# Performance work log

Measured on AMD Instinct MI355X. Metric: run time of the kernel, lower is better.

The kernel has to match this reference:

```python
import jax, jax.numpy as jnp
import numpy as np
import math

EPS = 1e-5

def _ln(x):
    # LayerNorm over last dim, no affine (elementwise_affine=False)
    m = jnp.mean(x, axis=-1, keepdims=True)
    v = jnp.var(x, axis=-1, keepdims=True)
    return (x - m) / jnp.sqrt(v + EPS)

def setup_inputs() -> dict:
    key = jax.random.key(0)
    ks = jax.random.split(key, 12)
    bs, P, L, D, H, V = 32, 256, 32, 128, 128, 300
    std = 1.0 / math.sqrt(H)
    xav = math.sqrt(2.0 / ((V + 1) + D))
    emb = jax.random.normal(ks[2], (V + 1, D), jnp.float32) * xav
    emb = emb.at[V].set(0.0)  # padding_idx row
    u = lambda k, shp: jax.random.uniform(k, shp, jnp.float32, -std, std)
    return {
        "paths": jax.random.randint(ks[0], (bs, P, L), 0, V + 1),
        "paths_mask": jax.random.randint(ks[1], (bs, P), 1, L + 1),
        "emb": emb,
        "Wi": u(ks[3], (2 * H, D)), "bi": u(ks[4], (2 * H,)),
        "Wh": u(ks[5], (2 * H, H)), "bh": u(ks[6], (2 * H,)),
        "Ww": u(ks[7], (H, D)), "bw": u(ks[8], (H,)),
        "Wu": u(ks[9], (H, H)), "bu": u(ks[10], (H,)),
        "gamma": jnp.ones((2 * H,), jnp.float32),
        "beta": jnp.zeros((2 * H,), jnp.float32),
    }

def reference(paths, paths_mask, emb, Wi, bi, Wh, bh, Ww, bw, Wu, bu, gamma, beta):
    bs, P, L = paths.shape
    D = emb.shape[1]
    H = Ww.shape[0]
    B = bs * P
    # Embed and flatten paths: [L, B, D] (time-major for scan)
    x = emb[paths].reshape(B * L and (B, L, D))  # [B, L, D]
    x = jnp.transpose(x, (1, 0, 2))              # [L, B, D]
    # Input-dependent parts precomputed across all timesteps
    xi = _ln(jnp.einsum('lbd,gd->lbg', x, Wi) + bi)  # [L, B, 2H]
    xw = _ln(jnp.einsum('lbd,hd->lbh', x, Ww) + bw)  # [L, B, H]

    def step(h, xs_t):
        i2h_t, xw_t = xs_t
        h2h = _ln(h @ Wh.T + bh)
        gates = jax.nn.sigmoid(i2h_t + h2h)
        z = gates[:, :H]
        r = gates[:, H:]
        hu = _ln(h @ Wu.T + bu)
        h_hat = jnp.tanh(xw_t + r * hu)
        h_new = (1.0 - z) * h + z * h_hat
        return h_new, h_new

    h0 = jnp.zeros((B, H), x.dtype)
    _, ys = jax.lax.scan(step, h0, (xi, xw))      # ys: [L, B, H]
    lengths = paths_mask.reshape(-1)              # [B]
    out = ys[lengths - 1, jnp.arange(B)]          # [B, H] hidden at last valid step
    out = out.reshape(bs, P, H)
    # interleave forward/backward halves (relation-path pairing)
    fwd = jnp.concatenate([out[:, 0::2, :], out[:, 1::2, :]], axis=-1)
    bwd = jnp.concatenate([out[:, 1::2, :], out[:, 0::2, :]], axis=-1)
    res = jnp.zeros((bs, P, 2 * H), out.dtype)
    res = res.at[:, 0::2, :].set(fwd).at[:, 1::2, :].set(bwd)
    # final affine LayerNorm (gru_ln)
    m = jnp.mean(res, axis=-1, keepdims=True)
    v = jnp.var(res, axis=-1, keepdims=True)
    return (res - m) / jnp.sqrt(v + EPS) * gamma + beta
```

## Files before the change

kernel.cpp:

```cpp
#include <hip/hip_runtime.h>

typedef float  f32x4 __attribute__((ext_vector_type(4)));
typedef short  s16x8 __attribute__((ext_vector_type(8)));

__device__ __forceinline__ unsigned short bfb(float x) {
  unsigned u = __builtin_bit_cast(unsigned, x);
  return (unsigned short)((u + 0x7FFFu + ((u >> 16) & 1u)) >> 16);
}
__device__ __forceinline__ float fast_sig(float x) {
  float e = __builtin_amdgcn_exp2f(x * -1.44269504f);
  return __builtin_amdgcn_rcpf(1.f + e);
}
__device__ __forceinline__ float fast_tanh(float x) {
  float e = __builtin_amdgcn_exp2f(x * 2.88539008f);
  return 1.f - 2.f * __builtin_amdgcn_rcpf(1.f + e);
}

__global__ __launch_bounds__(256) void tab_kernel(
    const float* __restrict__ emb,
    const float* __restrict__ Wi, const float* __restrict__ bi,
    const float* __restrict__ Ww, const float* __restrict__ bw,
    const float* __restrict__ Wh, const float* __restrict__ Wu,
    const int* __restrict__ pmask, int* __restrict__ perm,
    float* __restrict__ xi_tab, float* __restrict__ xw_tab,
    s16x8* __restrict__ frags)
{
  if (blockIdx.x == 309) {
    __shared__ int hist[33];
    __shared__ int base2[33];
    const int tid = threadIdx.x;
    if (tid < 33) hist[tid] = 0;
    __syncthreads();
    for (int i = tid; i < 8192; i += 256) atomicAdd(&hist[pmask[i]], 1);
    __syncthreads();
    if (tid == 0) {
      int acc = 0;
      for (int l = 1; l <= 32; ++l) { base2[l] = acc; acc += hist[l]; }
    }
    __syncthreads();
    for (int i = tid; i < 8192; i += 256) {
      const int pos = atomicAdd(&base2[pmask[i]], 1);
      perm[pos] = i;
    }
    return;
  }
  if (blockIdx.x >= 301) {
    const int T = blockIdx.x - 301;
    const int lane = threadIdx.x;
    if (lane >= 64) return;
    const int a = lane & 15, s = lane >> 4;
    const float* rowp[3];
    rowp[0] = Wh + (16 * T + a) * 128;
    rowp[1] = Wh + (128 + 16 * T + a) * 128;
    rowp[2] = Wu + (16 * T + a) * 128;
    #pragma unroll
    for (int mat = 0; mat < 3; ++mat) {
      #pragma unroll
      for (int kk = 0; kk < 4; ++kk) {
        const float* src = rowp[mat] + 32 * kk + 8 * s;
        const float4 A = *(const float4*)src;
        const float4 B = *(const float4*)(src + 4);
        s16x8 v;
        v[0] = (short)bfb(A.x); v[1] = (short)bfb(A.y);
        v[2] = (short)bfb(A.z); v[3] = (short)bfb(A.w);
        v[4] = (short)bfb(B.x); v[5] = (short)bfb(B.y);
        v[6] = (short)bfb(B.z); v[7] = (short)bfb(B.w);
        frags[((mat * 8 + T) * 4 + kk) * 64 + lane] = v;
      }
    }
    return;
  }

  const int v = blockIdx.x;
  const int g = threadIdx.x;
  const float4* er = (const float4*)(emb + v * 128);

  float acc = bi[g];
  const float4* wr = (const float4*)(Wi + g * 128);
  #pragma unroll 8
  for (int j = 0; j < 32; ++j) {
    float4 e = er[j], w4 = wr[j];
    acc = fmaf(e.x, w4.x, acc); acc = fmaf(e.y, w4.y, acc);
    acc = fmaf(e.z, w4.z, acc); acc = fmaf(e.w, w4.w, acc);
  }
  float accw = 0.f;
  if (g < 128) {
    accw = bw[g];
    const float4* wr2 = (const float4*)(Ww + g * 128);
    #pragma unroll 8
    for (int j = 0; j < 32; ++j) {
      float4 e = er[j], w4 = wr2[j];
      accw = fmaf(e.x, w4.x, accw); accw = fmaf(e.y, w4.y, accw);
      accw = fmaf(e.z, w4.z, accw); accw = fmaf(e.w, w4.w, accw);
    }
  }
  __shared__ float rs[4][2], rw[2][2];
  float s = acc, q = acc * acc;
  #pragma unroll
  for (int m = 1; m < 64; m <<= 1) { s += __shfl_xor(s, m); q += __shfl_xor(q, m); }
  if ((threadIdx.x & 63) == 0) { rs[threadIdx.x >> 6][0] = s; rs[threadIdx.x >> 6][1] = q; }
  float sw_ = accw, qw_ = accw * accw;
  #pragma unroll
  for (int m = 1; m < 64; m <<= 1) { sw_ += __shfl_xor(sw_, m); qw_ += __shfl_xor(qw_, m); }
  if (g < 128 && (g & 63) == 0) { rw[g >> 6][0] = sw_; rw[g >> 6][1] = qw_; }
  __syncthreads();
  const float SH = rs[0][0] + rs[1][0] + rs[2][0] + rs[3][0];
  const float QH = rs[0][1] + rs[1][1] + rs[2][1] + rs[3][1];
  const float mH = SH * (1.f / 256.f);
  const float rH = rsqrtf(fmaxf(QH * (1.f / 256.f) - mH * mH, 0.f) + 1e-5f);
  xi_tab[v * 256 + g] = (acc - mH) * rH;
  if (g < 128) {
    const float SW = rw[0][0] + rw[1][0], QW = rw[0][1] + rw[1][1];
    const float mW = SW * (1.f / 128.f);
    const float rW = rsqrtf(fmaxf(QW * (1.f / 128.f) - mW * mW, 0.f) + 1e-5f);
    xw_tab[v * 128 + g] = (accw - mW) * rW;
  }
}

__global__ __launch_bounds__(256, 2) void rec_kernel(
    const int* __restrict__ paths, const int* __restrict__ pmask,
    const int* __restrict__ perm,
    const float* __restrict__ bh, const float* __restrict__ bu,
    const float* __restrict__ xi_tab, const float* __restrict__ xw_tab,
    const s16x8* __restrict__ frags,
    float* __restrict__ out)
{
  __shared__ unsigned char hbuf[4096];
  __shared__ alignas(16) float red[4][4][16][4];
  __shared__ int plT[512];

  const int tid  = threadIdx.x;
  const int w    = tid >> 6;
  const int lane = tid & 63;
  const int s    = lane >> 4;
  const int r    = lane & 15;
  const int grp  = (blockIdx.x < 256) ? blockIdx.x : 767 - blockIdx.x;
  const int base = grp * 16;
  const int gb0  = 32 * w + 4 * s;

  s16x8 wz[2][4], wr2[2][4], wu2[2][4];
  #pragma unroll
  for (int u = 0; u < 2; ++u) {
    const int T = 2 * w + u;
    #pragma unroll
    for (int kk = 0; kk < 4; ++kk) {
      wz[u][kk]  = frags[((0 * 8 + T) * 4 + kk) * 64 + lane];
      wr2[u][kk] = frags[((1 * 8 + T) * 4 + kk) * 64 + lane];
      wu2[u][kk] = frags[((2 * 8 + T) * 4 + kk) * 64 + lane];
    }
  }

  for (int k = tid; k < 512; k += 256)
    plT[(k >> 4) * 16 + (k & 15)] = paths[perm[base + (k & 15)] * 32 + (k >> 4)];
  ((uint4*)hbuf)[tid] = uint4{0u, 0u, 0u, 0u};

  const int ri  = perm[base + r];
  const int len = pmask[ri];
  const int len_max = __shfl(len, 15);

  f32x4 bz[2], br2[2], bu2[2];
  #pragma unroll
  for (int u = 0; u < 2; ++u) {
    bz[u]  = *(const f32x4*)(bh + gb0 + 16 * u);
    br2[u] = *(const f32x4*)(bh + 128 + gb0 + 16 * u);
    bu2[u] = *(const f32x4*)(bu + gb0 + 16 * u);
  }

  int hoff[4];
  #pragma unroll
  for (int kk = 0; kk < 4; ++kk)
    hoff[kk] = r * 256 + (((4 * kk + s) ^ r) << 4);
  int hwadr[2];
  #pragma unroll
  for (int u = 0; u < 2; ++u)
    hwadr[u] = r * 256 + (((4 * w + 2 * u + (s >> 1)) ^ r) << 4) + (s & 1) * 8;

  float hreg[2][4] = {{0.f, 0.f, 0.f, 0.f}, {0.f, 0.f, 0.f, 0.f}};
  float* orow = out + (size_t)ri * 256 + gb0;

  __syncthreads();

  f32x4 xiz[2], xir[2], xwv[2];
  {
    const int p = plT[r];
    #pragma unroll
    for (int u = 0; u < 2; ++u) {
      xiz[u] = *(const f32x4*)(xi_tab + p * 256 + gb0 + 16 * u);
      xir[u] = *(const f32x4*)(xi_tab + p * 256 + 128 + gb0 + 16 * u);
      xwv[u] = *(const f32x4*)(xw_tab + p * 128 + gb0 + 16 * u);
    }
  }

  #pragma unroll 1
  for (int t = 0; t < len_max; ++t) {
    const int tn = (t + 1 < len_max) ? t + 1 : t;
    const int pn = plT[tn * 16 + r];
    f32x4 nxiz[2], nxir[2], nxwv[2];
    #pragma unroll
    for (int u = 0; u < 2; ++u) {
      nxiz[u] = *(const f32x4*)(xi_tab + pn * 256 + gb0 + 16 * u);
      nxir[u] = *(const f32x4*)(xi_tab + pn * 256 + 128 + gb0 + 16 * u);
      nxwv[u] = *(const f32x4*)(xw_tab + pn * 128 + gb0 + 16 * u);
    }

    f32x4 az[2] = {}, ar[2] = {}, au[2] = {};
    #pragma unroll
    for (int kk = 0; kk < 4; ++kk) {
      const s16x8 hb = *(const s16x8*)(hbuf + hoff[kk]);
      #pragma unroll
      for (int u = 0; u < 2; ++u) {
        az[u] = __builtin_amdgcn_mfma_f32_16x16x32_bf16(wz[u][kk],  hb, az[u], 0, 0, 0);
        ar[u] = __builtin_amdgcn_mfma_f32_16x16x32_bf16(wr2[u][kk], hb, ar[u], 0, 0, 0);
        au[u] = __builtin_amdgcn_mfma_f32_16x16x32_bf16(wu2[u][kk], hb, au[u], 0, 0, 0);
      }
    }

    float sH = 0.f, qH = 0.f, sU = 0.f, qU = 0.f;
    #pragma unroll
    for (int u = 0; u < 2; ++u) {
      #pragma unroll
      for (int i = 0; i < 4; ++i) {
        az[u][i] += bz[u][i];  sH += az[u][i]; qH = fmaf(az[u][i], az[u][i], qH);
        ar[u][i] += br2[u][i]; sH += ar[u][i]; qH = fmaf(ar[u][i], ar[u][i], qH);
        au[u][i] += bu2[u][i]; sU += au[u][i]; qU = fmaf(au[u][i], au[u][i], qU);
      }
    }
    *(f32x4*)&red[w][s][r][0] = f32x4{sH, qH, sU, qU};

    __syncthreads();

    f32x4 acc0 = *(const f32x4*)&red[0][0][r][0];
    f32x4 acc1 = *(const f32x4*)&red[0][1][r][0];
    #pragma unroll
    for (int c = 2; c < 16; c += 2) {
      acc0 += *(const f32x4*)&red[c >> 2][c & 3][r][0];
      acc1 += *(const f32x4*)&red[(c + 1) >> 2][(c + 1) & 3][r][0];
    }
    const f32x4 S = acc0 + acc1;
    const float mH = S[0] * (1.f / 256.f);
    const float rsH = rsqrtf(fmaxf(S[1] * (1.f / 256.f) - mH * mH, 0.f) + 1e-5f);
    const float cH = -mH * rsH;
    const float mU = S[2] * (1.f / 128.f);
    const float rsU = rsqrtf(fmaxf(S[3] * (1.f / 128.f) - mU * mU, 0.f) + 1e-5f);
    const float cU = -mU * rsU;

    float hn[2][4];
    #pragma unroll
    for (int u = 0; u < 2; ++u) {
      #pragma unroll
      for (int i = 0; i < 4; ++i) {
        const float zg = fast_sig(xiz[u][i] + fmaf(az[u][i], rsH, cH));
        const float rg = fast_sig(xir[u][i] + fmaf(ar[u][i], rsH, cH));
        const float hu = fmaf(au[u][i], rsU, cU);
        const float hh = fast_tanh(fmaf(rg, hu, xwv[u][i]));
        hn[u][i] = fmaf(zg, hh - hreg[u][i], hreg[u][i]);
      }
    }
    if (t == len - 1) {
      #pragma unroll
      for (int u = 0; u < 2; ++u)
        *(float4*)(orow + 16 * u) = float4{hn[u][0], hn[u][1], hn[u][2], hn[u][3]};
    }

    #pragma unroll
    for (int u = 0; u < 2; ++u) {
      const unsigned lo  = (unsigned)bfb(hn[u][0]) | ((unsigned)bfb(hn[u][1]) << 16);
      const unsigned hi2 = (unsigned)bfb(hn[u][2]) | ((unsigned)bfb(hn[u][3]) << 16);
      *(uint2*)(hbuf + hwadr[u]) = uint2{lo, hi2};
      #pragma unroll
      for (int i = 0; i < 4; ++i) hreg[u][i] = hn[u][i];
      xiz[u] = nxiz[u]; xir[u] = nxir[u]; xwv[u] = nxwv[u];
    }
    __syncthreads();
  }
}

__global__ __launch_bounds__(256) void out_kernel(
    const float* __restrict__ gamma, const float* __restrict__ beta,
    float* __restrict__ out)
{
  const int tid = threadIdx.x;
  const int lane = tid & 63;
  const int m = blockIdx.x * 4 + (tid >> 6);
  float* pa = out + (size_t)(2 * m) * 256;
  float* pb = pa + 256;
  const float oa0 = pa[lane], oa1 = pa[64 + lane];
  const float ob0 = pb[lane], ob1 = pb[64 + lane];
  float s = oa0 + oa1 + ob0 + ob1;
  float q = oa0 * oa0 + oa1 * oa1 + ob0 * ob0 + ob1 * ob1;
  #pragma unroll
  for (int msk = 1; msk < 64; msk <<= 1) { s += __shfl_xor(s, msk); q += __shfl_xor(q, msk); }
  const float mean = s * (1.f / 256.f);
  const float rstd = rsqrtf(fmaxf(q * (1.f / 256.f) - mean * mean, 0.f) + 1e-5f);
  const float g0 = gamma[lane], g1 = gamma[64 + lane], g2 = gamma[128 + lane], g3 = gamma[192 + lane];
  const float b0 = beta[lane],  b1 = beta[64 + lane],  b2 = beta[128 + lane],  b3 = beta[192 + lane];
  const float na0 = (oa0 - mean) * rstd, na1 = (oa1 - mean) * rstd;
  const float nb0 = (ob0 - mean) * rstd, nb1 = (ob1 - mean) * rstd;
  pa[lane]       = na0 * g0 + b0;
  pa[64 + lane]  = na1 * g1 + b1;
  pa[128 + lane] = nb0 * g2 + b2;
  pa[192 + lane] = nb1 * g3 + b3;
  pb[lane]       = nb0 * g0 + b0;
  pb[64 + lane]  = nb1 * g1 + b1;
  pb[128 + lane] = na0 * g2 + b2;
  pb[192 + lane] = na1 * g3 + b3;
}

extern "C" void kernel_launch(void* const* d_in, const int* in_sizes, int n_in,
                              void* d_out, int out_size, void* d_ws, size_t ws_size,
                              hipStream_t stream) {
  const int*   paths = (const int*)d_in[0];
  const int*   pmask = (const int*)d_in[1];
  const float* emb   = (const float*)d_in[2];
  const float* Wi    = (const float*)d_in[3];
  const float* bi    = (const float*)d_in[4];
  const float* Wh    = (const float*)d_in[5];
  const float* bh    = (const float*)d_in[6];
  const float* Ww    = (const float*)d_in[7];
  const float* bw    = (const float*)d_in[8];
  const float* Wu    = (const float*)d_in[9];
  const float* bu    = (const float*)d_in[10];
  const float* gamma = (const float*)d_in[11];
  const float* beta  = (const float*)d_in[12];
  float* out = (float*)d_out;

  float* xi_tab = (float*)d_ws;
  float* xw_tab = xi_tab + 301 * 256;
  s16x8* frags  = (s16x8*)((char*)d_ws + 462336);
  int*   perm   = (int*)((char*)d_ws + 560640);

  hipLaunchKernelGGL(tab_kernel, dim3(310), dim3(256), 0, stream,
                     emb, Wi, bi, Ww, bw, Wh, Wu, pmask, perm, xi_tab, xw_tab, frags);
  hipLaunchKernelGGL(rec_kernel, dim3(512), dim3(256), 0, stream,
                     paths, pmask, perm, bh, bu, xi_tab, xw_tab, frags, out);
  hipLaunchKernelGGL(out_kernel, dim3(1024), dim3(256), 0, stream, gamma, beta, out);
}
```

Baseline: 75.17 us.

## Run GRU recurrence with one wavefront per block, weights split between registers and LDS

Each 16-path group is now handled by a single 64-lane wavefront instead of four. Wu fragments stay in registers, while the Wh z/r fragments are staged in LDS and read every step. The LayerNorm reduction moves from shared memory plus block barriers to wave shuffles, removing per-step __syncthreads. The trade-off is that each wave issues four times as many MFMAs serially per step, the xi/xw prefetch for the next step is gone, and 73 KB of LDS per block limits how many blocks fit on a CU.

```diff
diff --git a/kernel.cpp b/kernel.cpp
--- a/kernel.cpp
+++ b/kernel.cpp
@@ -2,6 +2,8 @@
 
 typedef float  f32x4 __attribute__((ext_vector_type(4)));
 typedef short  s16x8 __attribute__((ext_vector_type(8)));
+
+#define REC_LDS_BYTES 73216
 
 __device__ __forceinline__ unsigned short bfb(float x) {
   unsigned u = __builtin_bit_cast(unsigned, x);
@@ -117,7 +119,7 @@
   }
 }
 
-__global__ __launch_bounds__(256, 2) void rec_kernel(
+__global__ __launch_bounds__(64, 1) void rec_kernel(
     const int* __restrict__ paths, const int* __restrict__ pmask,
     const int* __restrict__ perm,
     const float* __restrict__ bh, const float* __restrict__ bu,
@@ -125,153 +127,142 @@
     const s16x8* __restrict__ frags,
     float* __restrict__ out)
 {
-  __shared__ unsigned char hbuf[4096];
-  __shared__ alignas(16) float red[4][4][16][4];
-  __shared__ int plT[512];
-
-  const int tid  = threadIdx.x;
-  const int w    = tid >> 6;
-  const int lane = tid & 63;
+  extern __shared__ char smem[];
+  s16x8* wlds = (s16x8*)smem;
+  unsigned char* hbuf = (unsigned char*)(smem + 65536);
+  float* blds = (float*)(smem + 69632);
+  int* plT = (int*)(smem + 71168);
+
+  const int lane = threadIdx.x;
   const int s    = lane >> 4;
   const int r    = lane & 15;
   const int grp  = (blockIdx.x < 256) ? blockIdx.x : 767 - blockIdx.x;
   const int base = grp * 16;
-  const int gb0  = 32 * w + 4 * s;
-
-  s16x8 wz[2][4], wr2[2][4], wu2[2][4];
-  #pragma unroll
-  for (int u = 0; u < 2; ++u) {
-    const int T = 2 * w + u;
-    #pragma unroll
-    for (int kk = 0; kk < 4; ++kk) {
-      wz[u][kk]  = frags[((0 * 8 + T) * 4 + kk) * 64 + lane];
-      wr2[u][kk] = frags[((1 * 8 + T) * 4 + kk) * 64 + lane];
-      wu2[u][kk] = frags[((2 * 8 + T) * 4 + kk) * 64 + lane];
-    }
-  }
-
-  for (int k = tid; k < 512; k += 256)
+
+  #pragma unroll 4
+  for (int i = 0; i < 64; ++i)
+    wlds[i * 64 + lane] = frags[i * 64 + lane];
+  s16x8 wu[8][4];
+  #pragma unroll
+  for (int T = 0; T < 8; ++T)
+    #pragma unroll
+    for (int kk = 0; kk < 4; ++kk)
+      wu[T][kk] = frags[((16 + T) * 4 + kk) * 64 + lane];
+  #pragma unroll
+  for (int i = 0; i < 4; ++i) blds[lane + 64 * i] = bh[lane + 64 * i];
+  #pragma unroll
+  for (int i = 0; i < 2; ++i) blds[256 + lane + 64 * i] = bu[lane + 64 * i];
+  {
+    uint4 z{0u, 0u, 0u, 0u};
+    #pragma unroll
+    for (int i = 0; i < 4; ++i) ((uint4*)hbuf)[i * 64 + lane] = z;
+  }
+  #pragma unroll
+  for (int k0 = 0; k0 < 512; k0 += 64) {
+    const int k = k0 + lane;
     plT[(k >> 4) * 16 + (k & 15)] = paths[perm[base + (k & 15)] * 32 + (k >> 4)];
-  ((uint4*)hbuf)[tid] = uint4{0u, 0u, 0u, 0u};
+  }
 
   const int ri  = perm[base + r];
   const int len = pmask[ri];
   const int len_max = __shfl(len, 15);
 
-  f32x4 bz[2], br2[2], bu2[2];
-  #pragma unroll
-  for (int u = 0; u < 2; ++u) {
-    bz[u]  = *(const f32x4*)(bh + gb0 + 16 * u);
-    br2[u] = *(const f32x4*)(bh + 128 + gb0 + 16 * u);
-    bu2[u] = *(const f32x4*)(bu + gb0 + 16 * u);
-  }
-
   int hoff[4];
   #pragma unroll
   for (int kk = 0; kk < 4; ++kk)
     hoff[kk] = r * 256 + (((4 * kk + s) ^ r) << 4);
-  int hwadr[2];
-  #pragma unroll
-  for (int u = 0; u < 2; ++u)
-    hwadr[u] = r * 256 + (((4 * w + 2 * u + (s >> 1)) ^ r) << 4) + (s & 1) * 8;
-
-  float hreg[2][4] = {{0.f, 0.f, 0.f, 0.f}, {0.f, 0.f, 0.f, 0.f}};
-  float* orow = out + (size_t)ri * 256 + gb0;
-
-  __syncthreads();
-
-  f32x4 xiz[2], xir[2], xwv[2];
-  {
-    const int p = plT[r];
-    #pragma unroll
-    for (int u = 0; u < 2; ++u) {
-      xiz[u] = *(const f32x4*)(xi_tab + p * 256 + gb0 + 16 * u);
-      xir[u] = *(const f32x4*)(xi_tab + p * 256 + 128 + gb0 + 16 * u);
-      xwv[u] = *(const f32x4*)(xw_tab + p * 128 + gb0 + 16 * u);
-    }
-  }
+  int hwadr[8];
+  #pragma unroll
+  for (int T = 0; T < 8; ++T)
+    hwadr[T] = r * 256 + (((2 * T + (s >> 1)) ^ r) << 4) + (s & 1) * 8;
+
+  f32x4 hold[8];
+  #pragma unroll
+  for (int T = 0; T < 8; ++T) hold[T] = f32x4{0.f, 0.f, 0.f, 0.f};
+
+  float* orow = out + (size_t)ri * 256 + 4 * s;
 
   #pragma unroll 1
   for (int t = 0; t < len_max; ++t) {
-    const int tn = (t + 1 < len_max) ? t + 1 : t;
-    const int pn = plT[tn * 16 + r];
-    f32x4 nxiz[2], nxir[2], nxwv[2];
-    #pragma unroll
-    for (int u = 0; u < 2; ++u) {
-      nxiz[u] = *(const f32x4*)(xi_tab + pn * 256 + gb0 + 16 * u);
-      nxir[u] = *(const f32x4*)(xi_tab + pn * 256 + 128 + gb0 + 16 * u);
-      nxwv[u] = *(const f32x4*)(xw_tab + pn * 128 + gb0 + 16 * u);
-    }
-
-    f32x4 az[2] = {}, ar[2] = {}, au[2] = {};
-    #pragma unroll
-    for (int kk = 0; kk < 4; ++kk) {
-      const s16x8 hb = *(const s16x8*)(hbuf + hoff[kk]);
-      #pragma unroll
-      for (int u = 0; u < 2; ++u) {
-        az[u] = __builtin_amdgcn_mfma_f32_16x16x32_bf16(wz[u][kk],  hb, az[u], 0, 0, 0);
-        ar[u] = __builtin_amdgcn_mfma_f32_16x16x32_bf16(wr2[u][kk], hb, ar[u], 0, 0, 0);
-        au[u] = __builtin_amdgcn_mfma_f32_16x16x32_bf16(wu2[u][kk], hb, au[u], 0, 0, 0);
+    const int p = plT[t * 16 + r];
+
+    s16x8 hb[4];
+    #pragma unroll
+    for (int kk = 0; kk < 4; ++kk)
+      hb[kk] = *(const s16x8*)(hbuf + hoff[kk]);
+
+    f32x4 az[8], ar[8], au[8];
+    #pragma unroll
+    for (int T = 0; T < 8; ++T) {
+      az[T] = *(const f32x4*)&blds[16 * T + 4 * s];
+      ar[T] = *(const f32x4*)&blds[128 + 16 * T + 4 * s];
+      au[T] = *(const f32x4*)&blds[256 + 16 * T + 4 * s];
+    }
+    #pragma unroll
+    for (int kk = 0; kk < 4; ++kk)
+      #pragma unroll
+      for (int T = 0; T < 8; ++T)
+        au[T] = __builtin_amdgcn_mfma_f32_16x16x32_bf16(wu[T][kk], hb[kk], au[T], 0, 0, 0);
+    #pragma unroll
+    for (int T = 0; T < 8; ++T)
+      #pragma unroll
+      for (int kk = 0; kk < 4; ++kk)
+        az[T] = __builtin_amdgcn_mfma_f32_16x16x32_bf16(wlds[(T * 4 + kk) * 64 + lane], hb[kk], az[T], 0, 0, 0);
+    #pragma unroll
+    for (int T = 0; T < 8; ++T)
+      #pragma unroll
+      for (int kk = 0; kk < 4; ++kk)
+        ar[T] = __builtin_amdgcn_mfma_f32_16x16x32_bf16(wlds[((8 + T) * 4 + kk) * 64 + lane], hb[kk], ar[T], 0, 0, 0);
+
+    f32x4 xiz[8], xir[8], xwv[8];
+    #pragma unroll
+    for (int T = 0; T < 8; ++T) {
+      xiz[T] = *(const f32x4*)(xi_tab + p * 256 + 16 * T + 4 * s);
+      xir[T] = *(const f32x4*)(xi_tab + p * 256 + 128 + 16 * T + 4 * s);
+      xwv[T] = *(const f32x4*)(xw_tab + p * 128 + 16 * T + 4 * s);
+    }
+
+    float sH = 0.f, qH = 0.f, sU = 0.f, qU = 0.f;
+    #pragma unroll
+    for (int T = 0; T < 8; ++T) {
+      #pragma unroll
+      for (int i = 0; i < 4; ++i) {
+        sH += az[T][i]; qH = fmaf(az[T][i], az[T][i], qH);
+        sH += ar[T][i]; qH = fmaf(ar[T][i], ar[T][i], qH);
+        sU += au[T][i]; qU = fmaf(au[T][i], au[T][i], qU);
       }
     }
-
-    float sH = 0.f, qH = 0.f, sU = 0.f, qU = 0.f;
-    #pragma unroll
-    for (int u = 0; u < 2; ++u) {
+    sH += __shfl_xor(sH, 16); qH += __shfl_xor(qH, 16);
+    sU += __shfl_xor(sU, 16); qU += __shfl_xor(qU, 16);
+    sH += __shfl_xor(sH, 32); qH += __shfl_xor(qH, 32);
+    sU += __shfl_xor(sU, 32); qU += __shfl_xor(qU, 32);
+
+    const float mH = sH * (1.f / 256.f);
+    const float rsH = rsqrtf(fmaxf(qH * (1.f / 256.f) - mH * mH, 0.f) + 1e-5f);
+    const float cH = -mH * rsH;
+    const float mU = sU * (1.f / 128.f);
+    const float rsU = rsqrtf(fmaxf(qU * (1.f / 128.f) - mU * mU, 0.f) + 1e-5f);
+    const float cU = -mU * rsU;
+
+    const bool emit = (t == len - 1);
+    #pragma unroll
+    for (int T = 0; T < 8; ++T) {
+      f32x4 hn;
       #pragma unroll
       for (int i = 0; i < 4; ++i) {
-        az[u][i] += bz[u][i];  sH += az[u][i]; qH = fmaf(az[u][i], az[u][i], qH);
-        ar[u][i] += br2[u][i]; sH += ar[u][i]; qH = fmaf(ar[u][i], ar[u][i], qH);
-        au[u][i] += bu2[u][i]; sU += au[u][i]; qU = fmaf(au[u][i], au[u][i], qU);
+        const float zg = fast_sig(xiz[T][i] + fmaf(az[T][i], rsH, cH));
+        const float rg = fast_sig(xir[T][i] + fmaf(ar[T][i], rsH, cH));
+        const float hu = fmaf(au[T][i], rsU, cU);
+        const float hh = fast_tanh(fmaf(rg, hu, xwv[T][i]));
+        hn[i] = fmaf(zg, hh - hold[T][i], hold[T][i]);
       }
-    }
-    *(f32x4*)&red[w][s][r][0] = f32x4{sH, qH, sU, qU};
-
-    __syncthreads();
-
-    f32x4 acc0 = *(const f32x4*)&red[0][0][r][0];
-    f32x4 acc1 = *(const f32x4*)&red[0][1][r][0];
-    #pragma unroll
-    for (int c = 2; c < 16; c += 2) {
-      acc0 += *(const f32x4*)&red[c >> 2][c & 3][r][0];
-      acc1 += *(const f32x4*)&red[(c + 1) >> 2][(c + 1) & 3][r][0];
-    }
-    const f32x4 S = acc0 + acc1;
-    const float mH = S[0] * (1.f / 256.f);
-    const float rsH = rsqrtf(fmaxf(S[1] * (1.f / 256.f) - mH * mH, 0.f) + 1e-5f);
-    const float cH = -mH * rsH;
-    const float mU = S[2] * (1.f / 128.f);
-    const float rsU = rsqrtf(fmaxf(S[3] * (1.f / 128.f) - mU * mU, 0.f) + 1e-5f);
-    const float cU = -mU * rsU;
-
-    float hn[2][4];
-    #pragma unroll
-    for (int u = 0; u < 2; ++u) {
-      #pragma unroll
-      for (int i = 0; i < 4; ++i) {
-        const float zg = fast_sig(xiz[u][i] + fmaf(az[u][i], rsH, cH));
-        const float rg = fast_sig(xir[u][i] + fmaf(ar[u][i], rsH, cH));
-        const float hu = fmaf(au[u][i], rsU, cU);
-        const float hh = fast_tanh(fmaf(rg, hu, xwv[u][i]));
-        hn[u][i] = fmaf(zg, hh - hreg[u][i], hreg[u][i]);
-      }
-    }
-    if (t == len - 1) {
-      #pragma unroll
-      for (int u = 0; u < 2; ++u)
-        *(float4*)(orow + 16 * u) = float4{hn[u][0], hn[u][1], hn[u][2], hn[u][3]};
-    }
-
-    #pragma unroll
-    for (int u = 0; u < 2; ++u) {
-      const unsigned lo  = (unsigned)bfb(hn[u][0]) | ((unsigned)bfb(hn[u][1]) << 16);
-      const unsigned hi2 = (unsigned)bfb(hn[u][2]) | ((unsigned)bfb(hn[u][3]) << 16);
-      *(uint2*)(hbuf + hwadr[u]) = uint2{lo, hi2};
-      #pragma unroll
-      for (int i = 0; i < 4; ++i) hreg[u][i] = hn[u][i];
-      xiz[u] = nxiz[u]; xir[u] = nxir[u]; xwv[u] = nxwv[u];
-    }
-    __syncthreads();
+      const unsigned lo  = (unsigned)bfb(hn[0]) | ((unsigned)bfb(hn[1]) << 16);
+      const unsigned hi2 = (unsigned)bfb(hn[2]) | ((unsigned)bfb(hn[3]) << 16);
+      *(uint2*)(hbuf + hwadr[T]) = uint2{lo, hi2};
+      if (emit)
+        *(float4*)(orow + 16 * T) = float4{hn[0], hn[1], hn[2], hn[3]};
+      hold[T] = hn;
+    }
   }
 }
 
@@ -329,9 +320,12 @@
   s16x8* frags  = (s16x8*)((char*)d_ws + 462336);
   int*   perm   = (int*)((char*)d_ws + 560640);
 
+  hipFuncSetAttribute((const void*)rec_kernel,
+                      hipFuncAttributeMaxDynamicSharedMemorySize, REC_LDS_BYTES);
+
   hipLaunchKernelGGL(tab_kernel, dim3(310), dim3(256), 0, stream,
                      emb, Wi, bi, Ww, bw, Wh, Wu, pmask, perm, xi_tab, xw_tab, frags);
-  hipLaunchKernelGGL(rec_kernel, dim3(512), dim3(256), 0, stream,
+  hipLaunchKernelGGL(rec_kernel, dim3(512), dim3(64), REC_LDS_BYTES, stream,
                      paths, pmask, perm, bh, bu, xi_tab, xw_tab, frags, out);
   hipLaunchKernelGGL(out_kernel, dim3(1024), dim3(256), 0, stream, gamma, beta, out);
 }
```

Result: slower. 158.9 us (+111.4%).

## Interleave two independent 16-row groups per block to overlap MFMA with gate math

Applied to the files above, without the earlier changes.

Each recurrence block now processes two independent groups of 16 sequences in a ping-pong schedule with double-buffered hidden state and reduction buffers. The MFMA matmul and stats for one group are issued while the gate/LayerNorm finish of the other runs, hiding the serial dependency latency within a single block. The LayerNorm partial sums are now pre-reduced across the wave with shuffles, so only one lane group writes to shared memory. The grid is halved to 256 blocks with launch bounds of one block per SM. This trades cross-block occupancy for intra-block ILP, and each block now runs for the longest length across 32 rows instead of 16, which can add idle steps.

```diff
diff --git a/kernel.cpp b/kernel.cpp
--- a/kernel.cpp
+++ b/kernel.cpp
@@ -117,7 +117,84 @@
   }
 }
 
-__global__ __launch_bounds__(256, 2) void rec_kernel(
+__device__ __forceinline__ void mfma_stats(
+    const unsigned char* hbufg, float* redg ,
+    const int (&hoff)[4],
+    const s16x8 (&wz)[2][4], const s16x8 (&wr2)[2][4], const s16x8 (&wu2)[2][4],
+    const f32x4 (&bz)[2], const f32x4 (&br2)[2], const f32x4 (&bu2)[2],
+    int lane, int r,
+    f32x4 (&az)[2], f32x4 (&ar)[2], f32x4 (&au)[2])
+{
+  s16x8 hb[4];
+  #pragma unroll
+  for (int kk = 0; kk < 4; ++kk) hb[kk] = *(const s16x8*)(hbufg + hoff[kk]);
+  #pragma unroll
+  for (int u = 0; u < 2; ++u) {
+    az[u] = f32x4{0.f, 0.f, 0.f, 0.f}; ar[u] = az[u]; au[u] = az[u];
+  }
+  #pragma unroll
+  for (int kk = 0; kk < 4; ++kk) {
+    #pragma unroll
+    for (int u = 0; u < 2; ++u) {
+      az[u] = __builtin_amdgcn_mfma_f32_16x16x32_bf16(wz[u][kk],  hb[kk], az[u], 0, 0, 0);
+      ar[u] = __builtin_amdgcn_mfma_f32_16x16x32_bf16(wr2[u][kk], hb[kk], ar[u], 0, 0, 0);
+      au[u] = __builtin_amdgcn_mfma_f32_16x16x32_bf16(wu2[u][kk], hb[kk], au[u], 0, 0, 0);
+    }
+  }
+  float sH = 0.f, qH = 0.f, sU = 0.f, qU = 0.f;
+  #pragma unroll
+  for (int u = 0; u < 2; ++u) {
+    #pragma unroll
+    for (int i = 0; i < 4; ++i) {
+      az[u][i] += bz[u][i];  sH += az[u][i]; qH = fmaf(az[u][i], az[u][i], qH);
+      ar[u][i] += br2[u][i]; sH += ar[u][i]; qH = fmaf(ar[u][i], ar[u][i], qH);
+      au[u][i] += bu2[u][i]; sU += au[u][i]; qU = fmaf(au[u][i], au[u][i], qU);
+    }
+  }
+  sH += __shfl_xor(sH, 16); qH += __shfl_xor(qH, 16);
+  sU += __shfl_xor(sU, 16); qU += __shfl_xor(qU, 16);
+  sH += __shfl_xor(sH, 32); qH += __shfl_xor(qH, 32);
+  sU += __shfl_xor(sU, 32); qU += __shfl_xor(qU, 32);
+  if (lane < 16) *(f32x4*)&redg[r * 4] = f32x4{sH, qH, sU, qU};
+}
+
+__device__ __forceinline__ void finish_step(
+    const float* redb , int r,
+    f32x4 (&az)[2], f32x4 (&ar)[2], f32x4 (&au)[2],
+    const f32x4 (&xiz)[2], const f32x4 (&xir)[2], const f32x4 (&xwv)[2],
+    f32x4 (&hold)[2], unsigned char* hbufg, const int (&hwadr)[2],
+    float* orow, bool emit)
+{
+  f32x4 S = *(const f32x4*)&redb[r * 4];
+  #pragma unroll
+  for (int ww = 1; ww < 4; ++ww) S += *(const f32x4*)&redb[(ww * 16 + r) * 4];
+  const float mH = S[0] * (1.f / 256.f);
+  const float rsH = rsqrtf(fmaxf(S[1] * (1.f / 256.f) - mH * mH, 0.f) + 1e-5f);
+  const float cH = -mH * rsH;
+  const float mU = S[2] * (1.f / 128.f);
+  const float rsU = rsqrtf(fmaxf(S[3] * (1.f / 128.f) - mU * mU, 0.f) + 1e-5f);
+  const float cU = -mU * rsU;
+  #pragma unroll
+  for (int u = 0; u < 2; ++u) {
+    f32x4 hn;
+    #pragma unroll
+    for (int i = 0; i < 4; ++i) {
+      const float zg = fast_sig(xiz[u][i] + fmaf(az[u][i], rsH, cH));
+      const float rg = fast_sig(xir[u][i] + fmaf(ar[u][i], rsH, cH));
+      const float hu = fmaf(au[u][i], rsU, cU);
+      const float hh = fast_tanh(fmaf(rg, hu, xwv[u][i]));
+      hn[i] = fmaf(zg, hh - hold[u][i], hold[u][i]);
+    }
+    const unsigned lo  = (unsigned)bfb(hn[0]) | ((unsigned)bfb(hn[1]) << 16);
+    const unsigned hi2 = (unsigned)bfb(hn[2]) | ((unsigned)bfb(hn[3]) << 16);
+    *(uint2*)(hbufg + hwadr[u]) = uint2{lo, hi2};
+    if (emit)
+      *(float4*)(orow + 16 * u) = float4{hn[0], hn[1], hn[2], hn[3]};
+    hold[u] = hn;
+  }
+}
+
+__global__ __launch_bounds__(256, 1) void rec_kernel(
     const int* __restrict__ paths, const int* __restrict__ pmask,
     const int* __restrict__ perm,
     const float* __restrict__ bh, const float* __restrict__ bu,
@@ -125,17 +202,16 @@
     const s16x8* __restrict__ frags,
     float* __restrict__ out)
 {
-  __shared__ unsigned char hbuf[4096];
-  __shared__ alignas(16) float red[4][4][16][4];
-  __shared__ int plT[512];
+  __shared__ alignas(16) unsigned char hbuf[2][4096];
+  __shared__ alignas(16) float red[2][4][16][4];
+  __shared__ int plT[2][32][16];
 
   const int tid  = threadIdx.x;
   const int w    = tid >> 6;
   const int lane = tid & 63;
   const int s    = lane >> 4;
   const int r    = lane & 15;
-  const int grp  = (blockIdx.x < 256) ? blockIdx.x : 767 - blockIdx.x;
-  const int base = grp * 16;
+  const int base = blockIdx.x * 32;
   const int gb0  = 32 * w + 4 * s;
 
   s16x8 wz[2][4], wr2[2][4], wu2[2][4];
@@ -149,14 +225,16 @@
       wu2[u][kk] = frags[((2 * 8 + T) * 4 + kk) * 64 + lane];
     }
   }
-
-  for (int k = tid; k < 512; k += 256)
-    plT[(k >> 4) * 16 + (k & 15)] = paths[perm[base + (k & 15)] * 32 + (k >> 4)];
+  for (int k = tid; k < 1024; k += 256)
+    plT[k >> 9][(k >> 4) & 31][k & 15] = paths[perm[base + 16 * (k >> 9) + (k & 15)] * 32 + ((k >> 4) & 31)];
   ((uint4*)hbuf)[tid] = uint4{0u, 0u, 0u, 0u};
-
-  const int ri  = perm[base + r];
-  const int len = pmask[ri];
-  const int len_max = __shfl(len, 15);
+  ((uint4*)hbuf)[256 + tid] = uint4{0u, 0u, 0u, 0u};
+
+  const int riA  = perm[base + r];
+  const int riB  = perm[base + 16 + r];
+  const int lenA = pmask[riA];
+  const int lenB = pmask[riB];
+  const int len_max = __shfl(lenB, 15);
 
   f32x4 bz[2], br2[2], bu2[2];
   #pragma unroll
@@ -165,7 +243,6 @@
     br2[u] = *(const f32x4*)(bh + 128 + gb0 + 16 * u);
     bu2[u] = *(const f32x4*)(bu + gb0 + 16 * u);
   }
-
   int hoff[4];
   #pragma unroll
   for (int kk = 0; kk < 4; ++kk)
@@ -175,101 +252,65 @@
   for (int u = 0; u < 2; ++u)
     hwadr[u] = r * 256 + (((4 * w + 2 * u + (s >> 1)) ^ r) << 4) + (s & 1) * 8;
 
-  float hreg[2][4] = {{0.f, 0.f, 0.f, 0.f}, {0.f, 0.f, 0.f, 0.f}};
-  float* orow = out + (size_t)ri * 256 + gb0;
+  f32x4 holdA[2] = {f32x4{0.f,0.f,0.f,0.f}, f32x4{0.f,0.f,0.f,0.f}};
+  f32x4 holdB[2] = {f32x4{0.f,0.f,0.f,0.f}, f32x4{0.f,0.f,0.f,0.f}};
+  float* orowA = out + (size_t)riA * 256 + gb0;
+  float* orowB = out + (size_t)riB * 256 + gb0;
+
+  f32x4 azA[2], arA[2], auA[2], azB[2], arB[2], auB[2];
+  f32x4 xizA[2], xirA[2], xwvA[2], xizB[2], xirB[2], xwvB[2];
 
   __syncthreads();
 
-  f32x4 xiz[2], xir[2], xwv[2];
   {
-    const int p = plT[r];
+    const int pA = plT[0][0][r], pB = plT[1][0][r];
     #pragma unroll
     for (int u = 0; u < 2; ++u) {
-      xiz[u] = *(const f32x4*)(xi_tab + p * 256 + gb0 + 16 * u);
-      xir[u] = *(const f32x4*)(xi_tab + p * 256 + 128 + gb0 + 16 * u);
-      xwv[u] = *(const f32x4*)(xw_tab + p * 128 + gb0 + 16 * u);
-    }
-  }
+      xizA[u] = *(const f32x4*)(xi_tab + pA * 256 + gb0 + 16 * u);
+      xirA[u] = *(const f32x4*)(xi_tab + pA * 256 + 128 + gb0 + 16 * u);
+      xwvA[u] = *(const f32x4*)(xw_tab + pA * 128 + gb0 + 16 * u);
+      xizB[u] = *(const f32x4*)(xi_tab + pB * 256 + gb0 + 16 * u);
+      xirB[u] = *(const f32x4*)(xi_tab + pB * 256 + 128 + gb0 + 16 * u);
+      xwvB[u] = *(const f32x4*)(xw_tab + pB * 128 + gb0 + 16 * u);
+    }
+  }
+  mfma_stats(hbuf[0], &red[0][w][0][0], hoff, wz, wr2, wu2, bz, br2, bu2, lane, r, azA, arA, auA);
+  __syncthreads();
 
   #pragma unroll 1
   for (int t = 0; t < len_max; ++t) {
     const int tn = (t + 1 < len_max) ? t + 1 : t;
-    const int pn = plT[tn * 16 + r];
-    f32x4 nxiz[2], nxir[2], nxwv[2];
-    #pragma unroll
-    for (int u = 0; u < 2; ++u) {
-      nxiz[u] = *(const f32x4*)(xi_tab + pn * 256 + gb0 + 16 * u);
-      nxir[u] = *(const f32x4*)(xi_tab + pn * 256 + 128 + gb0 + 16 * u);
-      nxwv[u] = *(const f32x4*)(xw_tab + pn * 128 + gb0 + 16 * u);
-    }
-
-    f32x4 az[2] = {}, ar[2] = {}, au[2] = {};
-    #pragma unroll
-    for (int kk = 0; kk < 4; ++kk) {
-      const s16x8 hb = *(const s16x8*)(hbuf + hoff[kk]);
+    mfma_stats(hbuf[1], &red[1][w][0][0], hoff, wz, wr2, wu2, bz, br2, bu2, lane, r, azB, arB, auB);
+    {
+      const int pA = plT[0][tn][r];
+      f32x4 nxiz[2], nxir[2], nxwv[2];
       #pragma unroll
       for (int u = 0; u < 2; ++u) {
-        az[u] = __builtin_amdgcn_mfma_f32_16x16x32_bf16(wz[u][kk],  hb, az[u], 0, 0, 0);
-        ar[u] = __builtin_amdgcn_mfma_f32_16x16x32_bf16(wr2[u][kk], hb, ar[u], 0, 0, 0);
-        au[u] = __builtin_amdgcn_mfma_f32_16x16x32_bf16(wu2[u][kk], hb, au[u], 0, 0, 0);
+        nxiz[u] = *(const f32x4*)(xi_tab + pA * 256 + gb0 + 16 * u);
+        nxir[u] = *(const f32x4*)(xi_tab + pA * 256 + 128 + gb0 + 16 * u);
+        nxwv[u] = *(const f32x4*)(xw_tab + pA * 128 + gb0 + 16 * u);
       }
-    }
-
-    float sH = 0.f, qH = 0.f, sU = 0.f, qU = 0.f;
-    #pragma unroll
-    for (int u = 0; u < 2; ++u) {
-      #pragma unroll
-      for (int i = 0; i < 4; ++i) {
-        az[u][i] += bz[u][i];  sH += az[u][i]; qH = fmaf(az[u][i], az[u][i], qH);
-        ar[u][i] += br2[u][i]; sH += ar[u][i]; qH = fmaf(ar[u][i], ar[u][i], qH);
-        au[u][i] += bu2[u][i]; sU += au[u][i]; qU = fmaf(au[u][i], au[u][i], qU);
+      finish_step(&red[0][0][0][0], r, azA, arA, auA, xizA, xirA, xwvA,
+                  holdA, hbuf[0], hwadr, orowA, t == lenA - 1);
+      #pragma unroll
+      for (int u = 0; u < 2; ++u) { xizA[u] = nxiz[u]; xirA[u] = nxir[u]; xwvA[u] = nxwv[u]; }
+    }
+    __syncthreads();
+    if (t + 1 < len_max)
+      mfma_stats(hbuf[0], &red[0][w][0][0], hoff, wz, wr2, wu2, bz, br2, bu2, lane, r, azA, arA, auA);
+    {
+      const int pB = plT[1][tn][r];
+      f32x4 nxiz[2], nxir[2], nxwv[2];
+      #pragma unroll
+      for (int u = 0; u < 2; ++u) {
+        nxiz[u] = *(const f32x4*)(xi_tab + pB * 256 + gb0 + 16 * u);
+        nxir[u] = *(const f32x4*)(xi_tab + pB * 256 + 128 + gb0 + 16 * u);
+        nxwv[u] = *(const f32x4*)(xw_tab + pB * 128 + gb0 + 16 * u);
       }
-    }
-    *(f32x4*)&red[w][s][r][0] = f32x4{sH, qH, sU, qU};
-
-    __syncthreads();
-
-    f32x4 acc0 = *(const f32x4*)&red[0][0][r][0];
-    f32x4 acc1 = *(const f32x4*)&red[0][1][r][0];
-    #pragma unroll
-    for (int c = 2; c < 16; c += 2) {
-      acc0 += *(const f32x4*)&red[c >> 2][c & 3][r][0];
-      acc1 += *(const f32x4*)&red[(c + 1) >> 2][(c + 1) & 3][r][0];
-    }
-    const f32x4 S = acc0 + acc1;
-    const float mH = S[0] * (1.f / 256.f);
-    const float rsH = rsqrtf(fmaxf(S[1] * (1.f / 256.f) - mH * mH, 0.f) + 1e-5f);
-    const float cH = -mH * rsH;
-    const float mU = S[2] * (1.f / 128.f);
-    const float rsU = rsqrtf(fmaxf(S[3] * (1.f / 128.f) - mU * mU, 0.f) + 1e-5f);
-    const float cU = -mU * rsU;
-
-    float hn[2][4];
-    #pragma unroll
-    for (int u = 0; u < 2; ++u) {
-      #pragma unroll
-      for (int i = 0; i < 4; ++i) {
-        const float zg = fast_sig(xiz[u][i] + fmaf(az[u][i], rsH, cH));
-        const float rg = fast_sig(xir[u][i] + fmaf(ar[u][i], rsH, cH));
-        const float hu = fmaf(au[u][i], rsU, cU);
-        const float hh = fast_tanh(fmaf(rg, hu, xwv[u][i]));
-        hn[u][i] = fmaf(zg, hh - hreg[u][i], hreg[u][i]);
-      }
-    }
-    if (t == len - 1) {
-      #pragma unroll
-      for (int u = 0; u < 2; ++u)
-        *(float4*)(orow + 16 * u) = float4{hn[u][0], hn[u][1], hn[u][2], hn[u][3]};
-    }
-
-    #pragma unroll
-    for (int u = 0; u < 2; ++u) {
-      const unsigned lo  = (unsigned)bfb(hn[u][0]) | ((unsigned)bfb(hn[u][1]) << 16);
-      const unsigned hi2 = (unsigned)bfb(hn[u][2]) | ((unsigned)bfb(hn[u][3]) << 16);
-      *(uint2*)(hbuf + hwadr[u]) = uint2{lo, hi2};
-      #pragma unroll
-      for (int i = 0; i < 4; ++i) hreg[u][i] = hn[u][i];
-      xiz[u] = nxiz[u]; xir[u] = nxir[u]; xwv[u] = nxwv[u];
+      finish_step(&red[1][0][0][0], r, azB, arB, auB, xizB, xirB, xwvB,
+                  holdB, hbuf[1], hwadr, orowB, t == lenB - 1);
+      #pragma unroll
+      for (int u = 0; u < 2; ++u) { xizB[u] = nxiz[u]; xirB[u] = nxir[u]; xwvB[u] = nxwv[u]; }
     }
     __syncthreads();
   }
@@ -331,7 +372,7 @@
 
   hipLaunchKernelGGL(tab_kernel, dim3(310), dim3(256), 0, stream,
                      emb, Wi, bi, Ww, bw, Wh, Wu, pmask, perm, xi_tab, xw_tab, frags);
-  hipLaunchKernelGGL(rec_kernel, dim3(512), dim3(256), 0, stream,
+  hipLaunchKernelGGL(rec_kernel, dim3(256), dim3(256), 0, stream,
                      paths, pmask, perm, bh, bu, xi_tab, xw_tab, frags, out);
   hipLaunchKernelGGL(out_kernel, dim3(1024), dim3(256), 0, stream, gamma, beta, out);
 }
```

New measurement: 119.4 us. +58.8%, slower.
